# Performance work log

Measured on AMD Instinct MI355X. Metric: run time of the kernel, lower is better.

The kernel has to match this reference:

```python
import jax, jax.numpy as jnp
import numpy as np

GAMMA = 2.0
K_NEIGH = 10
N = 8192
F_IN = 512     # recon_fea_dim
F_HID = 512    # graph_h_dim
F_OUT = 256    # graph_out_dim
N_CLU = 10     # cluster_num


def setup_inputs() -> dict:
    key = jax.random.key(0)
    ks = jax.random.split(key, 8)
    x = jax.random.normal(ks[0], (N, F_IN), dtype=jnp.float32)
    # GCN layer 1 (selu activation, skip connection)
    W1 = jax.random.normal(ks[1], (F_IN, F_HID), dtype=jnp.float32) * (1.0 / np.sqrt(F_IN))
    b1 = jnp.zeros((F_HID,), dtype=jnp.float32)
    skip1 = jnp.ones((F_HID,), dtype=jnp.float32)
    # GCN layer 2 (identity activation, skip connection)
    W2 = jax.random.normal(ks[2], (F_HID, F_OUT), dtype=jnp.float32) * (1.0 / np.sqrt(F_HID))
    b2 = jnp.zeros((F_OUT,), dtype=jnp.float32)
    skip2 = jnp.ones((F_OUT,), dtype=jnp.float32)
    # MGC transform: Linear(graph_out_dim -> n_clusters)
    Wt = jax.random.normal(ks[3], (N_CLU, F_OUT), dtype=jnp.float32) * (1.0 / np.sqrt(F_OUT))
    bt = jnp.zeros((N_CLU,), dtype=jnp.float32)
    return {"x": x, "W1": W1, "b1": b1, "skip1": skip1,
            "W2": W2, "b2": b2, "skip2": skip2, "Wt": Wt, "bt": bt}


def _build_knn_graph(x):
    # pairwise squared distance via gram trick (same math as (x_i - x_j)**2 sum)
    sq = jnp.sum(x * x, axis=1)                       # [N]
    d2 = sq[:, None] + sq[None, :] - 2.0 * (x @ x.T)  # [N, N]
    S = jnp.exp(-d2 / GAMMA)
    S = jnp.where(jnp.eye(S.shape[0], dtype=bool), -jnp.inf, S)
    _, idx = jax.lax.top_k(S, K_NEIGH)                # [N, K]
    n = S.shape[0]
    rows = jnp.broadcast_to(jnp.arange(n)[:, None], idx.shape)
    A = jnp.zeros((n, n), dtype=jnp.float32)
    A = A.at[rows, idx].set(1.0)
    A = A.at[idx, rows].set(1.0)                      # symmetrize
    rowsum = jnp.sum(A, axis=1)
    inv = jnp.where(rowsum > 0, 1.0 / rowsum, 0.0)
    A_hat = A * inv[:, None]                          # D^{-1} A
    return A, A_hat


def _gcn_layer(h, A_hat, W, b, skip, act):
    out = h @ W
    out = out * skip + A_hat @ out                    # fused skip + aggregation
    out = out + b
    return act(out)


def reference(x, W1, b1, skip1, W2, b2, skip2, Wt, bt):
    A, A_hat = _build_knn_graph(x)
    # GCN encode: gc1 (selu) -> relu -> gc2 (identity)
    h = _gcn_layer(x, A_hat, W1, b1, skip1, jax.nn.selu)
    h = jax.nn.relu(h)
    emb = _gcn_layer(h, A_hat, W2, b2, skip2, lambda v: v)  # [N, F_OUT]
    # MGC spectral clustering loss
    assign = jax.nn.softmax(emb @ Wt.T + bt, axis=1)  # [N, C]
    deg = jnp.sum(A, axis=0)[:, None]                 # [N, 1]
    n_edges = jnp.sum(deg)
    graph_pooled = (A @ assign).T @ assign            # [C, C]
    norm_l = assign.T @ deg                           # [C, 1]
    norm_r = deg.T @ assign                           # [1, C]
    normalizer = (norm_l @ norm_r) / 2.0 / n_edges
    spectral_loss = -jnp.trace(graph_pooled - normalizer) / 2.0 / n_edges
    return spectral_loss
```

## Files before the change

kernel.cpp:

```cpp
#include <hip/hip_runtime.h>
#include <math.h>
#include <stdint.h>

#define NPTS 8192
#define FIN 512
#define FHID 512
#define FOUT 256
#define NCLU 10
#define KNEI 10
#define GAMMA_F 2.0f
#define LISTCAP 4160

typedef __attribute__((ext_vector_type(4))) float f32x4;
typedef __attribute__((ext_vector_type(8))) short bf16x8;

__global__ void k_sumsq(const float* __restrict__ x, float* __restrict__ sq) {
    int row = blockIdx.x;
    const float* xr = x + (size_t)row * FIN;
    float s = 0.f;
    for (int k = threadIdx.x; k < FIN; k += 256) s += xr[k] * xr[k];
    __shared__ float red[256];
    red[threadIdx.x] = s; __syncthreads();
    for (int off = 128; off > 0; off >>= 1) {
        if (threadIdx.x < off) red[threadIdx.x] += red[threadIdx.x + off];
        __syncthreads();
    }
    if (threadIdx.x == 0) sq[row] = red[0];
}

__global__ void k_tobf16(const float* __restrict__ x, unsigned short* __restrict__ xb) {
    int i = blockIdx.x * 256 + threadIdx.x;
    f32x4 v = reinterpret_cast<const f32x4*>(x)[i];
    ushort4 o;
    #pragma unroll
    for (int e = 0; e < 4; e++) {
        union { float f; unsigned u; } cvt; cvt.f = v[e];
        unsigned r = (cvt.u + 0x7FFFu + ((cvt.u >> 16) & 1u)) >> 16;
        ((unsigned short*)&o)[e] = (unsigned short)r;
    }
    reinterpret_cast<ushort4*>(xb)[i] = o;
}

#define GR_ROWS 64
#define GR_TW 128
#define GR_CHUNKS 8
#define GR_CHUNK_COLS (NPTS / GR_CHUNKS)
#define GR_TILES_PER_CHUNK (GR_CHUNK_COLS / GR_TW)
#define GR_STEPS (GR_TILES_PER_CHUNK * 8)

__global__ __launch_bounds__(256, 3) void k_gram_topk(
    const unsigned short* __restrict__ xb, const float* __restrict__ sq,
    float* __restrict__ tpv, int* __restrict__ tpi)
{
    __shared__ short Bl[2][128][64];
    __shared__ float tval[GR_ROWS][KNEI];
    __shared__ int   tidxs[GR_ROWS][KNEI];

    const int tid  = threadIdx.x;
    const int lane = tid & 63;
    const int wv   = tid >> 6;
    const int rg   = blockIdx.x >> 3;
    const int ch   = blockIdx.x & 7;
    const int r0   = rg * GR_ROWS;
    const int cbase = ch * GR_CHUNK_COLS;

    for (int e = tid; e < GR_ROWS * KNEI; e += 256) {
        tval[e / KNEI][e % KNEI] = -INFINITY;
        tidxs[e / KNEI][e % KNEI] = 0x7fffffff;
    }

    const int arow  = r0 + wv * 16 + (lane & 15);
    const int akoff = (lane >> 4) * 8;
    bf16x8 afr[16];
    #pragma unroll
    for (int ks = 0; ks < 16; ks++)
        afr[ks] = *reinterpret_cast<const bf16x8*>(xb + (size_t)arow * FIN + ks * 32 + akoff);

    float si_r[4];
    #pragma unroll
    for (int r = 0; r < 4; r++) si_r[r] = sq[r0 + wv * 16 + (lane >> 4) * 4 + r];

    const int stg_row = tid >> 1, stg_seg = tid & 1;

    bf16x8 pre[4];
    {
        const unsigned short* src = xb + (size_t)(cbase + stg_row) * FIN + stg_seg * 32;
        #pragma unroll
        for (int q = 0; q < 4; q++) pre[q] = *reinterpret_cast<const bf16x8*>(src + q * 8);
        #pragma unroll
        for (int q = 0; q < 4; q++) {
            int kk8 = stg_seg * 4 + q;
            *reinterpret_cast<bf16x8*>(&Bl[0][stg_row][(kk8 ^ (stg_row & 7)) * 8]) = pre[q];
        }
    }
    __syncthreads();

    f32x4 acc[8];
    for (int u = 0; u < GR_STEPS; ++u) {
        const int t  = u >> 3, kc = u & 7;
        const int c0 = cbase + t * GR_TW;
        const int cur = u & 1;

        if (kc == 0) {
            #pragma unroll
            for (int ct = 0; ct < 8; ct++) acc[ct] = (f32x4){0.f, 0.f, 0.f, 0.f};
        }

        if (u < GR_STEPS - 1) {
            const int u2 = u + 1, t2 = u2 >> 3, kc2 = u2 & 7;
            const unsigned short* src = xb + (size_t)(cbase + t2 * GR_TW + stg_row) * FIN + kc2 * 64 + stg_seg * 32;
            #pragma unroll
            for (int q = 0; q < 4; q++) pre[q] = *reinterpret_cast<const bf16x8*>(src + q * 8);
        }

        #pragma unroll
        for (int ksl = 0; ksl < 2; ++ksl) {
            #pragma unroll
            for (int ct = 0; ct < 8; ct++) {
                const int cl = ct * 16 + (lane & 15);
                const int q = ksl * 4 + (lane >> 4);
                bf16x8 bfr = *reinterpret_cast<const bf16x8*>(&Bl[cur][cl][(q ^ (cl & 7)) * 8]);
                acc[ct] = __builtin_amdgcn_mfma_f32_16x16x32_bf16(afr[kc * 2 + ksl], bfr, acc[ct], 0, 0, 0);
            }
        }

        if (kc == 7) {
            #pragma unroll
            for (int ct = 0; ct < 8; ct++) {
                const int gj  = c0 + ct * 16 + (lane & 15);
                const float sjv = sq[gj];
                float sv[4];
                #pragma unroll
                for (int r = 0; r < 4; r++) {
                    const int gi = r0 + wv * 16 + (lane >> 4) * 4 + r;
                    const float d2 = si_r[r] + sjv - 2.f * acc[ct][r];
                    sv[r] = (gj == gi) ? -INFINITY : expf(-d2 * 0.5f);
                }
                #pragma unroll
                for (int r = 0; r < 4; r++) {
                    const int myrow = wv * 16 + (lane >> 4) * 4 + r;
                    float t9 = tval[myrow][KNEI - 1];
                    int   i9 = tidxs[myrow][KNEI - 1];
                    unsigned long long bal = __ballot(sv[r] > t9 || (sv[r] == t9 && gj < i9));
                    while (bal) {
                        int l = __ffsll(bal) - 1;
                        bal &= bal - 1;
                        float cv = __shfl(sv[r], l);
                        int   cj = c0 + ct * 16 + (l & 15);
                        int   rfull = wv * 16 + (l >> 4) * 4 + r;
                        if (lane == 0) {
                            float a9 = tval[rfull][KNEI - 1];
                            int   i9b = tidxs[rfull][KNEI - 1];
                            if (cv > a9 || (cv == a9 && cj < i9b)) {
                                int pp = KNEI - 1;
                                tval[rfull][pp] = cv; tidxs[rfull][pp] = cj;
                                while (pp > 0) {
                                    float pv = tval[rfull][pp - 1]; int pi = tidxs[rfull][pp - 1];
                                    if (cv > pv || (cv == pv && cj < pi)) {
                                        tval[rfull][pp] = pv; tidxs[rfull][pp] = pi;
                                        tval[rfull][pp - 1] = cv; tidxs[rfull][pp - 1] = cj;
                                        --pp;
                                    } else break;
                                }
                            }
                        }
                    }
                }
            }
        }

        if (u < GR_STEPS - 1) {
            #pragma unroll
            for (int q = 0; q < 4; q++) {
                int kk8 = stg_seg * 4 + q;
                *reinterpret_cast<bf16x8*>(&Bl[cur ^ 1][stg_row][(kk8 ^ (stg_row & 7)) * 8]) = pre[q];
            }
        }
        __syncthreads();
    }

    for (int e = tid; e < GR_ROWS * KNEI; e += 256) {
        int r = e / KNEI, m = e % KNEI;
        size_t o = (((size_t)(r0 + r) * GR_CHUNKS) + ch) * KNEI + m;
        tpv[o] = tval[r][m];
        tpi[o] = tidxs[r][m];
    }
}

__global__ __launch_bounds__(256) void k_topk_merge(const float* __restrict__ tpv,
        const int* __restrict__ tpi, int* __restrict__ topidx) {
    int r = blockIdx.x * 256 + threadIdx.x;
    int p[GR_CHUNKS];
    #pragma unroll
    for (int c = 0; c < GR_CHUNKS; c++) p[c] = 0;
    #pragma unroll
    for (int m = 0; m < KNEI; m++) {
        float bv = -INFINITY; int bi = 0x7fffffff; int bc = 0;
        #pragma unroll
        for (int c = 0; c < GR_CHUNKS; c++) {
            if (p[c] < KNEI) {
                size_t o = (((size_t)r * GR_CHUNKS) + c) * KNEI + p[c];
                float v = tpv[o];
                int idx = tpi[o];
                if (v > bv || (v == bv && idx < bi)) { bv = v; bi = idx; bc = c; }
            }
        }
        topidx[(size_t)r * KNEI + m] = bi;
        p[bc]++;
    }
}

__global__ void k_set_edges(const int* __restrict__ topidx, unsigned int* __restrict__ mask) {
    int t = blockIdx.x * 256 + threadIdx.x;
    if (t >= NPTS * KNEI) return;
    int i = t / KNEI;
    int j = topidx[t];
    atomicOr(&mask[(size_t)i * (NPTS / 32) + (j >> 5)], 1u << (j & 31));
    atomicOr(&mask[(size_t)j * (NPTS / 32) + (i >> 5)], 1u << (i & 31));
}

__global__ void k_degree(const unsigned int* __restrict__ mask, float* __restrict__ degf,
                         float* __restrict__ inv) {
    int i = blockIdx.x, lane = threadIdx.x;
    int c = 0;
    for (int w = lane; w < NPTS / 32; w += 64) c += __popc(mask[(size_t)i * (NPTS / 32) + w]);
    for (int off = 32; off > 0; off >>= 1) c += __shfl_xor(c, off);
    if (lane == 0) {
        float d = (float)c;
        degf[i] = d;
        inv[i] = (c > 0) ? 1.0f / d : 0.0f;
    }
}

__global__ __launch_bounds__(256) void k_gemm(const float* __restrict__ A, const float* __restrict__ B,
                                              float* __restrict__ C, int M, int Kd, int Nd) {
    __shared__ float Al[64][17];
    __shared__ float Bl[16][65];
    int tid = threadIdx.x;
    int bx = blockIdx.x, by = blockIdx.y;
    int tx = tid & 15, ty = tid >> 4;
    float acc[4][4];
    #pragma unroll
    for (int i = 0; i < 4; i++)
        #pragma unroll
        for (int j = 0; j < 4; j++) acc[i][j] = 0.f;

    for (int kt = 0; kt < Kd; kt += 16) {
        #pragma unroll
        for (int l = 0; l < 4; l++) {
            int e = tid + l * 256;
            int r = e >> 4, k = e & 15;
            Al[r][k] = A[(size_t)(by * 64 + r) * Kd + kt + k];
        }
        #pragma unroll
        for (int l = 0; l < 4; l++) {
            int e = tid + l * 256;
            int r = e >> 6, n = e & 63;
            Bl[r][n] = B[(size_t)(kt + r) * Nd + bx * 64 + n];
        }
        __syncthreads();
        #pragma unroll
        for (int k = 0; k < 16; k++) {
            float a[4], b[4];
            #pragma unroll
            for (int i = 0; i < 4; i++) a[i] = Al[ty * 4 + i][k];
            #pragma unroll
            for (int j = 0; j < 4; j++) b[j] = Bl[k][tx * 4 + j];
            #pragma unroll
            for (int i = 0; i < 4; i++)
                #pragma unroll
                for (int j = 0; j < 4; j++) acc[i][j] = fmaf(a[i], b[j], acc[i][j]);
        }
        __syncthreads();
    }
    #pragma unroll
    for (int i = 0; i < 4; i++)
        #pragma unroll
        for (int j = 0; j < 4; j++)
            C[(size_t)(by * 64 + ty * 4 + i) * Nd + bx * 64 + tx * 4 + j] = acc[i][j];
}

__global__ __launch_bounds__(256) void k_colsum(const float* __restrict__ P, float* __restrict__ colsum, int Fd) {
    int f = blockIdx.x * 256 + threadIdx.x;
    int r0 = blockIdx.y * (NPTS / 64);
    float s = 0.f;
    for (int r = 0; r < NPTS / 64; r++) s += P[(size_t)(r0 + r) * Fd + f];
    atomicAdd(&colsum[f], s);
}

template <int ACT>
__global__ __launch_bounds__(256) void k_aggregate(const float* __restrict__ P, float* __restrict__ OUT,
        const float* __restrict__ skip, const float* __restrict__ bias,
        const float* __restrict__ inv, const unsigned int* __restrict__ mask,
        const float* __restrict__ colsum, int Fd) {
    __shared__ unsigned short list[LISTCAP];
    __shared__ int cnt_total;
    __shared__ int pos;
    int i = blockIdx.x, tid = threadIdx.x;
    if (tid == 0) { cnt_total = 0; pos = 0; }
    __syncthreads();
    unsigned int w = mask[(size_t)i * (NPTS / 32) + tid];
    atomicAdd(&cnt_total, __popc(w));
    __syncthreads();
    const int deg = cnt_total;
    const bool comp = deg > 4096;
    unsigned int wm = comp ? ~w : w;
    if (comp && tid == (i >> 5)) wm &= ~(1u << (i & 31));
    while (wm) {
        int b = __ffs(wm) - 1;
        wm &= wm - 1;
        int pp = atomicAdd(&pos, 1);
        list[pp] = (unsigned short)(tid * 32 + b);
    }
    __syncthreads();
    const int n = comp ? (NPTS - 1 - deg) : deg;
    const float vinv = inv[i];
    for (int f = tid; f < Fd; f += 256) {
        float s = 0.f;
        for (int q = 0; q < n; q++) s += P[(size_t)list[q] * Fd + f];
        const float pif = P[(size_t)i * Fd + f];
        const float nb = comp ? (colsum[f] - pif - s) : s;
        float o = pif * skip[f] + vinv * nb + bias[f];
        if (ACT == 1) o = (o > 0.f) ? 1.0507009873554805f * o : 0.f;
        OUT[(size_t)i * Fd + f] = o;
    }
}

__global__ void k_assign(const float* __restrict__ emb, const float* __restrict__ Wt,
                         const float* __restrict__ bt, float* __restrict__ assign) {
    int i = blockIdx.x, lane = threadIdx.x;
    float e[4];
    #pragma unroll
    for (int m = 0; m < 4; m++) e[m] = emb[(size_t)i * FOUT + lane + 64 * m];
    float logit[NCLU];
    #pragma unroll
    for (int c = 0; c < NCLU; c++) {
        float p = 0.f;
        #pragma unroll
        for (int m = 0; m < 4; m++) p = fmaf(e[m], Wt[c * FOUT + lane + 64 * m], p);
        #pragma unroll
        for (int off = 32; off > 0; off >>= 1) p += __shfl_xor(p, off);
        logit[c] = p + bt[c];
    }
    float mx = logit[0];
    #pragma unroll
    for (int c = 1; c < NCLU; c++) mx = fmaxf(mx, logit[c]);
    float sum = 0.f, pr[NCLU];
    #pragma unroll
    for (int c = 0; c < NCLU; c++) { pr[c] = expf(logit[c] - mx); sum += pr[c]; }
    float isum = 1.f / sum;
    if (lane < NCLU) {
        float v = 0.f;
        #pragma unroll
        for (int c = 0; c < NCLU; c++) if (lane == c) v = pr[c];
        assign[(size_t)i * NCLU + lane] = v * isum;
    }
}

__global__ __launch_bounds__(256) void k_stats(const float* __restrict__ assign,
        const float* __restrict__ degf, float* __restrict__ colA,
        float* __restrict__ vvec, float* __restrict__ Esum) {
    __shared__ float sc[NCLU], sv[NCLU], se;
    int tid = threadIdx.x;
    if (tid < NCLU) { sc[tid] = 0.f; sv[tid] = 0.f; }
    if (tid == 0) se = 0.f;
    __syncthreads();
    int i = blockIdx.x * 256 + tid;
    const float d = degf[i];
    const float* ar = assign + (size_t)i * NCLU;
    float ed = d;
    #pragma unroll
    for (int off = 32; off > 0; off >>= 1) ed += __shfl_xor(ed, off);
    if ((tid & 63) == 0) atomicAdd(&se, ed);
    #pragma unroll
    for (int c = 0; c < NCLU; c++) {
        float a = ar[c];
        float av = a * d;
        #pragma unroll
        for (int off = 32; off > 0; off >>= 1) { a += __shfl_xor(a, off); av += __shfl_xor(av, off); }
        if ((tid & 63) == 0) { atomicAdd(&sc[c], a); atomicAdd(&sv[c], av); }
    }
    __syncthreads();
    if (tid < NCLU) { atomicAdd(&colA[tid], sc[tid]); atomicAdd(&vvec[tid], sv[tid]); }
    if (tid == NCLU) atomicAdd(Esum, se);
}

__global__ __launch_bounds__(256) void k_spectral(const unsigned int* __restrict__ mask,
        const float* __restrict__ assign, const float* __restrict__ colA,
        float* __restrict__ Tpart) {
    __shared__ unsigned short list[LISTCAP];
    __shared__ int cnt_total;
    __shared__ int pos;
    __shared__ float red[4][NCLU];
    int i = blockIdx.x, tid = threadIdx.x;
    if (tid == 0) { cnt_total = 0; pos = 0; }
    __syncthreads();
    unsigned int w = mask[(size_t)i * (NPTS / 32) + tid];
    atomicAdd(&cnt_total, __popc(w));
    __syncthreads();
    const int deg = cnt_total;
    const bool comp = deg > 4096;
    unsigned int wm = comp ? ~w : w;
    if (comp && tid == (i >> 5)) wm &= ~(1u << (i & 31));
    while (wm) {
        int b = __ffs(wm) - 1;
        wm &= wm - 1;
        int pp = atomicAdd(&pos, 1);
        list[pp] = (unsigned short)(tid * 32 + b);
    }
    __syncthreads();
    const int n = comp ? (NPTS - 1 - deg) : deg;
    float yc[NCLU];
    #pragma unroll
    for (int c = 0; c < NCLU; c++) yc[c] = 0.f;
    for (int q = tid; q < n; q += 256) {
        const float* aj = assign + (size_t)list[q] * NCLU;
        #pragma unroll
        for (int c = 0; c < NCLU; c++) yc[c] += aj[c];
    }
    #pragma unroll
    for (int c = 0; c < NCLU; c++) {
        #pragma unroll
        for (int off = 32; off > 0; off >>= 1) yc[c] += __shfl_xor(yc[c], off);
    }
    int wv = tid >> 6, lane = tid & 63;
    if (lane == 0) {
        #pragma unroll
        for (int c = 0; c < NCLU; c++) red[wv][c] = yc[c];
    }
    __syncthreads();
    if (tid == 0) {
        const float* ai = assign + (size_t)i * NCLU;
        float t = 0.f;
        #pragma unroll
        for (int c = 0; c < NCLU; c++) {
            float y = red[0][c] + red[1][c] + red[2][c] + red[3][c];
            if (comp) y = colA[c] - ai[c] - y;
            t = fmaf(y, ai[c], t);
        }
        Tpart[i] = t;
    }
}

__global__ __launch_bounds__(256) void k_final(const float* __restrict__ Tpart,
        const float* __restrict__ v, const float* __restrict__ Esum, float* __restrict__ out) {
    __shared__ float red[256];
    int tid = threadIdx.x;
    float s = 0.f;
    for (int i = tid; i < NPTS; i += 256) s += Tpart[i];
    red[tid] = s; __syncthreads();
    for (int off = 128; off > 0; off >>= 1) {
        if (tid < off) red[tid] += red[tid + off];
        __syncthreads();
    }
    if (tid == 0) {
        float E = *Esum;
        float v2 = 0.f;
        for (int c = 0; c < NCLU; c++) v2 += v[c] * v[c];
        float tr_norm = v2 / (2.f * E);
        out[0] = -(red[0] - tr_norm) / (2.f * E);
    }
}

extern "C" void kernel_launch(void* const* d_in, const int* in_sizes, int n_in,
                              void* d_out, int out_size, void* d_ws, size_t ws_size,
                              hipStream_t stream) {
    const float* x     = (const float*)d_in[0];
    const float* W1    = (const float*)d_in[1];
    const float* b1    = (const float*)d_in[2];
    const float* skip1 = (const float*)d_in[3];
    const float* W2    = (const float*)d_in[4];
    const float* b2    = (const float*)d_in[5];
    const float* skip2 = (const float*)d_in[6];
    const float* Wt    = (const float*)d_in[7];
    const float* bt    = (const float*)d_in[8];

    char* ws = (char*)d_ws;
    float* bufA = (float*)ws;
    float* bufB = (float*)(ws + ((size_t)16 << 20));
    unsigned int* mask = (unsigned int*)(ws + ((size_t)32 << 20));
    char* p = ws + ((size_t)40 << 20);
    float* sq     = (float*)p; p += NPTS * 4;
    float* degf   = (float*)p; p += NPTS * 4;
    float* inv    = (float*)p; p += NPTS * 4;
    int*   topidx = (int*)p;   p += (size_t)NPTS * KNEI * 4;
    float* assign = (float*)p; p += (size_t)NPTS * NCLU * 4;
    float* Tpart  = (float*)p; p += NPTS * 4;
    float* Esum    = (float*)p; p += 4;
    float* vvec    = (float*)p; p += NCLU * 4;
    float* colA    = (float*)p; p += NCLU * 4;
    float* colsum1 = (float*)p; p += FHID * 4;
    float* colsum2 = (float*)p; p += FOUT * 4;

    unsigned short* xb = (unsigned short*)bufA;
    float* tpv = (float*)bufB;
    int*   tpi = (int*)((char*)bufB + ((size_t)4 << 20));

    hipMemsetAsync(mask, 0, (size_t)NPTS * (NPTS / 32) * 4, stream);
    hipMemsetAsync(Esum, 0, (1 + 2 * NCLU + FHID + FOUT) * sizeof(float), stream);

    k_sumsq<<<NPTS, 256, 0, stream>>>(x, sq);
    k_tobf16<<<(NPTS * FIN / 4) / 256, 256, 0, stream>>>(x, xb);
    k_gram_topk<<<(NPTS / GR_ROWS) * GR_CHUNKS, 256, 0, stream>>>(xb, sq, tpv, tpi);
    k_topk_merge<<<NPTS / 256, 256, 0, stream>>>(tpv, tpi, topidx);
    k_set_edges<<<(NPTS * KNEI + 255) / 256, 256, 0, stream>>>(topidx, mask);
    k_degree<<<NPTS, 64, 0, stream>>>(mask, degf, inv);

    k_gemm<<<dim3(FHID / 64, NPTS / 64), 256, 0, stream>>>(x, W1, bufA, NPTS, FIN, FHID);
    k_colsum<<<dim3(FHID / 256, 64), 256, 0, stream>>>(bufA, colsum1, FHID);
    k_aggregate<1><<<NPTS, 256, 0, stream>>>(bufA, bufB, skip1, b1, inv, mask, colsum1, FHID);
    k_gemm<<<dim3(FOUT / 64, NPTS / 64), 256, 0, stream>>>(bufB, W2, bufA, NPTS, FHID, FOUT);
    k_colsum<<<dim3(FOUT / 256, 64), 256, 0, stream>>>(bufA, colsum2, FOUT);
    k_aggregate<0><<<NPTS, 256, 0, stream>>>(bufA, bufB, skip2, b2, inv, mask, colsum2, FOUT);

    k_assign<<<NPTS, 64, 0, stream>>>(bufB, Wt, bt, assign);
    k_stats<<<NPTS / 256, 256, 0, stream>>>(assign, degf, colA, vvec, Esum);
    k_spectral<<<NPTS, 256, 0, stream>>>(mask, assign, colA, Tpart);
    k_final<<<1, 256, 0, stream>>>(Tpart, vvec, Esum, (float*)d_out);
}
```

Before: 728.8 us.

## Use split-bf16 MFMA GEMMs for GCN layers and enlarge gram-topk row tile

The scalar fp32 shared-memory GEMMs for both GCN layers are replaced by an MFMA kernel. Each fp32 operand is split into high and low bf16 parts, and three bf16 MFMA products (hi*hi, hi*lo, lo*hi) give near-fp32 accuracy. New helper kernels split the activations and transpose and split the weights; B fragments are read directly from global memory with no LDS staging. Separately, the gram/top-k kernel now processes 128 rows per block with 512 threads, which amortizes B-tile staging over more rows. In exchange there are extra split passes, a dropped lo*lo term, and different occupancy in the gram kernel.

```diff
diff --git a/kernel.cpp b/kernel.cpp
--- a/kernel.cpp
+++ b/kernel.cpp
@@ -8,11 +8,19 @@
 #define FOUT 256
 #define NCLU 10
 #define KNEI 10
-#define GAMMA_F 2.0f
 #define LISTCAP 4160
 
 typedef __attribute__((ext_vector_type(4))) float f32x4;
 typedef __attribute__((ext_vector_type(8))) short bf16x8;
+
+__device__ __forceinline__ unsigned short bf16_rne(float f) {
+    union { float f; unsigned u; } c; c.f = f;
+    return (unsigned short)((c.u + 0x7FFFu + ((c.u >> 16) & 1u)) >> 16);
+}
+__device__ __forceinline__ float bf16_to_f(unsigned short h) {
+    union { unsigned u; float f; } c; c.u = ((unsigned)h) << 16;
+    return c.f;
+}
 
 __global__ void k_sumsq(const float* __restrict__ x, float* __restrict__ sq) {
     int row = blockIdx.x;
@@ -28,27 +36,48 @@
     if (threadIdx.x == 0) sq[row] = red[0];
 }
 
-__global__ void k_tobf16(const float* __restrict__ x, unsigned short* __restrict__ xb) {
+__global__ void k_split(const float* __restrict__ in, unsigned short* __restrict__ hi,
+                        unsigned short* __restrict__ lo) {
     int i = blockIdx.x * 256 + threadIdx.x;
-    f32x4 v = reinterpret_cast<const f32x4*>(x)[i];
-    ushort4 o;
+    f32x4 v = reinterpret_cast<const f32x4*>(in)[i];
+    ushort4 h, l;
     #pragma unroll
     for (int e = 0; e < 4; e++) {
-        union { float f; unsigned u; } cvt; cvt.f = v[e];
-        unsigned r = (cvt.u + 0x7FFFu + ((cvt.u >> 16) & 1u)) >> 16;
-        ((unsigned short*)&o)[e] = (unsigned short)r;
-    }
-    reinterpret_cast<ushort4*>(xb)[i] = o;
-}
-
-#define GR_ROWS 64
+        unsigned short hb = bf16_rne(v[e]);
+        ((unsigned short*)&h)[e] = hb;
+        ((unsigned short*)&l)[e] = bf16_rne(v[e] - bf16_to_f(hb));
+    }
+    reinterpret_cast<ushort4*>(hi)[i] = h;
+    reinterpret_cast<ushort4*>(lo)[i] = l;
+}
+
+__global__ __launch_bounds__(256) void k_wtrans(const float* __restrict__ W,
+        unsigned short* __restrict__ TH, unsigned short* __restrict__ TL, int K, int N) {
+    __shared__ float t[32][33];
+    int k0 = blockIdx.y * 32, n0 = blockIdx.x * 32;
+    int ln = threadIdx.x & 31, lt = threadIdx.x >> 5;
+    #pragma unroll
+    for (int q = 0; q < 4; q++)
+        t[lt + q * 8][ln] = W[(size_t)(k0 + lt + q * 8) * N + n0 + ln];
+    __syncthreads();
+    #pragma unroll
+    for (int q = 0; q < 4; q++) {
+        float v = t[ln][lt + q * 8];
+        unsigned short hb = bf16_rne(v);
+        size_t o = (size_t)(n0 + lt + q * 8) * K + k0 + ln;
+        TH[o] = hb;
+        TL[o] = bf16_rne(v - bf16_to_f(hb));
+    }
+}
+
+#define GR_ROWS 128
 #define GR_TW 128
 #define GR_CHUNKS 8
 #define GR_CHUNK_COLS (NPTS / GR_CHUNKS)
 #define GR_TILES_PER_CHUNK (GR_CHUNK_COLS / GR_TW)
 #define GR_STEPS (GR_TILES_PER_CHUNK * 8)
 
-__global__ __launch_bounds__(256, 3) void k_gram_topk(
+__global__ __launch_bounds__(512, 2) void k_gram_topk(
     const unsigned short* __restrict__ xb, const float* __restrict__ sq,
     float* __restrict__ tpv, int* __restrict__ tpi)
 {
@@ -64,7 +93,7 @@
     const int r0   = rg * GR_ROWS;
     const int cbase = ch * GR_CHUNK_COLS;
 
-    for (int e = tid; e < GR_ROWS * KNEI; e += 256) {
+    for (int e = tid; e < GR_ROWS * KNEI; e += 512) {
         tval[e / KNEI][e % KNEI] = -INFINITY;
         tidxs[e / KNEI][e % KNEI] = 0x7fffffff;
     }
@@ -80,17 +109,17 @@
     #pragma unroll
     for (int r = 0; r < 4; r++) si_r[r] = sq[r0 + wv * 16 + (lane >> 4) * 4 + r];
 
-    const int stg_row = tid >> 1, stg_seg = tid & 1;
-
-    bf16x8 pre[4];
+    const int stg_row = tid >> 2, stg_seg = tid & 3;
+
+    bf16x8 pre[2];
     {
-        const unsigned short* src = xb + (size_t)(cbase + stg_row) * FIN + stg_seg * 32;
-        #pragma unroll
-        for (int q = 0; q < 4; q++) pre[q] = *reinterpret_cast<const bf16x8*>(src + q * 8);
-        #pragma unroll
-        for (int q = 0; q < 4; q++) {
-            int kk8 = stg_seg * 4 + q;
-            *reinterpret_cast<bf16x8*>(&Bl[0][stg_row][(kk8 ^ (stg_row & 7)) * 8]) = pre[q];
+        const unsigned short* src = xb + (size_t)(cbase + stg_row) * FIN + stg_seg * 16;
+        #pragma unroll
+        for (int q = 0; q < 2; q++) pre[q] = *reinterpret_cast<const bf16x8*>(src + q * 8);
+        #pragma unroll
+        for (int q = 0; q < 2; q++) {
+            int g = stg_seg * 2 + q;
+            *reinterpret_cast<bf16x8*>(&Bl[0][stg_row][(g ^ (stg_row & 7)) * 8]) = pre[q];
         }
     }
     __syncthreads();
@@ -108,9 +137,9 @@
 
         if (u < GR_STEPS - 1) {
             const int u2 = u + 1, t2 = u2 >> 3, kc2 = u2 & 7;
-            const unsigned short* src = xb + (size_t)(cbase + t2 * GR_TW + stg_row) * FIN + kc2 * 64 + stg_seg * 32;
+            const unsigned short* src = xb + (size_t)(cbase + t2 * GR_TW + stg_row) * FIN + kc2 * 64 + stg_seg * 16;
             #pragma unroll
-            for (int q = 0; q < 4; q++) pre[q] = *reinterpret_cast<const bf16x8*>(src + q * 8);
+            for (int q = 0; q < 2; q++) pre[q] = *reinterpret_cast<const bf16x8*>(src + q * 8);
         }
 
         #pragma unroll
@@ -171,15 +200,15 @@
 
         if (u < GR_STEPS - 1) {
             #pragma unroll
-            for (int q = 0; q < 4; q++) {
-                int kk8 = stg_seg * 4 + q;
-                *reinterpret_cast<bf16x8*>(&Bl[cur ^ 1][stg_row][(kk8 ^ (stg_row & 7)) * 8]) = pre[q];
+            for (int q = 0; q < 2; q++) {
+                int g = stg_seg * 2 + q;
+                *reinterpret_cast<bf16x8*>(&Bl[cur ^ 1][stg_row][(g ^ (stg_row & 7)) * 8]) = pre[q];
             }
         }
         __syncthreads();
     }
 
-    for (int e = tid; e < GR_ROWS * KNEI; e += 256) {
+    for (int e = tid; e < GR_ROWS * KNEI; e += 512) {
         int r = e / KNEI, m = e % KNEI;
         size_t o = (((size_t)(r0 + r) * GR_CHUNKS) + ch) * KNEI + m;
         tpv[o] = tval[r][m];
@@ -232,52 +261,49 @@
     }
 }
 
-__global__ __launch_bounds__(256) void k_gemm(const float* __restrict__ A, const float* __restrict__ B,
-                                              float* __restrict__ C, int M, int Kd, int Nd) {
-    __shared__ float Al[64][17];
-    __shared__ float Bl[16][65];
-    int tid = threadIdx.x;
-    int bx = blockIdx.x, by = blockIdx.y;
-    int tx = tid & 15, ty = tid >> 4;
-    float acc[4][4];
-    #pragma unroll
-    for (int i = 0; i < 4; i++)
-        #pragma unroll
-        for (int j = 0; j < 4; j++) acc[i][j] = 0.f;
-
-    for (int kt = 0; kt < Kd; kt += 16) {
-        #pragma unroll
-        for (int l = 0; l < 4; l++) {
-            int e = tid + l * 256;
-            int r = e >> 4, k = e & 15;
-            Al[r][k] = A[(size_t)(by * 64 + r) * Kd + kt + k];
-        }
-        #pragma unroll
-        for (int l = 0; l < 4; l++) {
-            int e = tid + l * 256;
-            int r = e >> 6, n = e & 63;
-            Bl[r][n] = B[(size_t)(kt + r) * Nd + bx * 64 + n];
-        }
-        __syncthreads();
-        #pragma unroll
-        for (int k = 0; k < 16; k++) {
-            float a[4], b[4];
+__global__ __launch_bounds__(256) void k_gemm_mfma(
+    const unsigned short* __restrict__ Ahi, const unsigned short* __restrict__ Alo,
+    const unsigned short* __restrict__ BThi, const unsigned short* __restrict__ BTlo,
+    float* __restrict__ C, int M, int K, int N)
+{
+    const int tid = threadIdx.x, lane = tid & 63, wv = tid >> 6;
+    const int bx = blockIdx.x, by = blockIdx.y;
+    const int arow = by * 64 + wv * 16 + (lane & 15);
+    const int koff = (lane >> 4) * 8;
+
+    f32x4 acc[8];
+    #pragma unroll
+    for (int ct = 0; ct < 8; ct++) acc[ct] = (f32x4){0.f, 0.f, 0.f, 0.f};
+
+    for (int kb = 0; kb < K; kb += 128) {
+        bf16x8 ah[4], al[4];
+        #pragma unroll
+        for (int ksl = 0; ksl < 4; ksl++) {
+            ah[ksl] = *reinterpret_cast<const bf16x8*>(Ahi + (size_t)arow * K + kb + ksl * 32 + koff);
+            al[ksl] = *reinterpret_cast<const bf16x8*>(Alo + (size_t)arow * K + kb + ksl * 32 + koff);
+        }
+        #pragma unroll
+        for (int ksl = 0; ksl < 4; ksl++) {
             #pragma unroll
-            for (int i = 0; i < 4; i++) a[i] = Al[ty * 4 + i][k];
-            #pragma unroll
-            for (int j = 0; j < 4; j++) b[j] = Bl[k][tx * 4 + j];
-            #pragma unroll
-            for (int i = 0; i < 4; i++)
-                #pragma unroll
-                for (int j = 0; j < 4; j++) acc[i][j] = fmaf(a[i], b[j], acc[i][j]);
-        }
-        __syncthreads();
-    }
-    #pragma unroll
-    for (int i = 0; i < 4; i++)
-        #pragma unroll
-        for (int j = 0; j < 4; j++)
-            C[(size_t)(by * 64 + ty * 4 + i) * Nd + bx * 64 + tx * 4 + j] = acc[i][j];
+            for (int ct = 0; ct < 8; ct++) {
+                const int n = bx * 128 + ct * 16 + (lane & 15);
+                bf16x8 bh = *reinterpret_cast<const bf16x8*>(BThi + (size_t)n * K + kb + ksl * 32 + koff);
+                bf16x8 bl = *reinterpret_cast<const bf16x8*>(BTlo + (size_t)n * K + kb + ksl * 32 + koff);
+                acc[ct] = __builtin_amdgcn_mfma_f32_16x16x32_bf16(ah[ksl], bh, acc[ct], 0, 0, 0);
+                acc[ct] = __builtin_amdgcn_mfma_f32_16x16x32_bf16(ah[ksl], bl, acc[ct], 0, 0, 0);
+                acc[ct] = __builtin_amdgcn_mfma_f32_16x16x32_bf16(al[ksl], bh, acc[ct], 0, 0, 0);
+            }
+        }
+    }
+    #pragma unroll
+    for (int ct = 0; ct < 8; ct++) {
+        const int col = bx * 128 + ct * 16 + (lane & 15);
+        #pragma unroll
+        for (int r = 0; r < 4; r++) {
+            const int row = by * 64 + wv * 16 + (lane >> 4) * 4 + r;
+            C[(size_t)row * N + col] = acc[ct][r];
+        }
+    }
 }
 
 __global__ __launch_bounds__(256) void k_colsum(const float* __restrict__ P, float* __restrict__ colsum, int Fd) {
@@ -479,7 +505,8 @@
     float* bufA = (float*)ws;
     float* bufB = (float*)(ws + ((size_t)16 << 20));
     unsigned int* mask = (unsigned int*)(ws + ((size_t)32 << 20));
-    char* p = ws + ((size_t)40 << 20);
+    unsigned short* xlo = (unsigned short*)(ws + ((size_t)40 << 20));
+    char* p = ws + ((size_t)48 << 20);
     float* sq     = (float*)p; p += NPTS * 4;
     float* degf   = (float*)p; p += NPTS * 4;
     float* inv    = (float*)p; p += NPTS * 4;
@@ -491,29 +518,40 @@
     float* colA    = (float*)p; p += NCLU * 4;
     float* colsum1 = (float*)p; p += FHID * 4;
     float* colsum2 = (float*)p; p += FOUT * 4;
+    unsigned short* WT1hi = (unsigned short*)p; p += (size_t)FHID * FIN * 2;
+    unsigned short* WT1lo = (unsigned short*)p; p += (size_t)FHID * FIN * 2;
+    unsigned short* WT2hi = (unsigned short*)p; p += (size_t)FOUT * FHID * 2;
+    unsigned short* WT2lo = (unsigned short*)p; p += (size_t)FOUT * FHID * 2;
 
     unsigned short* xb = (unsigned short*)bufA;
     float* tpv = (float*)bufB;
     int*   tpi = (int*)((char*)bufB + ((size_t)4 << 20));
+    unsigned short* hhi = (unsigned short*)bufB;
+    float* P2 = bufB + ((size_t)2 << 20);
 
     hipMemsetAsync(mask, 0, (size_t)NPTS * (NPTS / 32) * 4, stream);
     hipMemsetAsync(Esum, 0, (1 + 2 * NCLU + FHID + FOUT) * sizeof(float), stream);
 
     k_sumsq<<<NPTS, 256, 0, stream>>>(x, sq);
-    k_tobf16<<<(NPTS * FIN / 4) / 256, 256, 0, stream>>>(x, xb);
-    k_gram_topk<<<(NPTS / GR_ROWS) * GR_CHUNKS, 256, 0, stream>>>(xb, sq, tpv, tpi);
+    k_split<<<(NPTS * FIN / 4) / 256, 256, 0, stream>>>(x, xb, xlo);
+    k_wtrans<<<dim3(FHID / 32, FIN / 32), 256, 0, stream>>>(W1, WT1hi, WT1lo, FIN, FHID);
+    k_wtrans<<<dim3(FOUT / 32, FHID / 32), 256, 0, stream>>>(W2, WT2hi, WT2lo, FHID, FOUT);
+
+    k_gram_topk<<<(NPTS / GR_ROWS) * GR_CHUNKS, 512, 0, stream>>>(xb, sq, tpv, tpi);
     k_topk_merge<<<NPTS / 256, 256, 0, stream>>>(tpv, tpi, topidx);
     k_set_edges<<<(NPTS * KNEI + 255) / 256, 256, 0, stream>>>(topidx, mask);
     k_degree<<<NPTS, 64, 0, stream>>>(mask, degf, inv);
 
-    k_gemm<<<dim3(FHID / 64, NPTS / 64), 256, 0, stream>>>(x, W1, bufA, NPTS, FIN, FHID);
-    k_colsum<<<dim3(FHID / 256, 64), 256, 0, stream>>>(bufA, colsum1, FHID);
-    k_aggregate<1><<<NPTS, 256, 0, stream>>>(bufA, bufB, skip1, b1, inv, mask, colsum1, FHID);
-    k_gemm<<<dim3(FOUT / 64, NPTS / 64), 256, 0, stream>>>(bufB, W2, bufA, NPTS, FHID, FOUT);
-    k_colsum<<<dim3(FOUT / 256, 64), 256, 0, stream>>>(bufA, colsum2, FOUT);
-    k_aggregate<0><<<NPTS, 256, 0, stream>>>(bufA, bufB, skip2, b2, inv, mask, colsum2, FOUT);
-
-    k_assign<<<NPTS, 64, 0, stream>>>(bufB, Wt, bt, assign);
+    k_gemm_mfma<<<dim3(FHID / 128, NPTS / 64), 256, 0, stream>>>(xb, xlo, WT1hi, WT1lo, bufB, NPTS, FIN, FHID);
+    k_colsum<<<dim3(FHID / 256, 64), 256, 0, stream>>>(bufB, colsum1, FHID);
+    k_aggregate<1><<<NPTS, 256, 0, stream>>>(bufB, bufA, skip1, b1, inv, mask, colsum1, FHID);
+
+    k_split<<<(NPTS * FHID / 4) / 256, 256, 0, stream>>>(bufA, hhi, xlo);
+    k_gemm_mfma<<<dim3(FOUT / 128, NPTS / 64), 256, 0, stream>>>(hhi, xlo, WT2hi, WT2lo, P2, NPTS, FHID, FOUT);
+    k_colsum<<<dim3(FOUT / 256, 64), 256, 0, stream>>>(P2, colsum2, FOUT);
+    k_aggregate<0><<<NPTS, 256, 0, stream>>>(P2, bufA, skip2, b2, inv, mask, colsum2, FOUT);
+
+    k_assign<<<NPTS, 64, 0, stream>>>(bufA, Wt, bt, assign);
     k_stats<<<NPTS / 256, 256, 0, stream>>>(assign, degf, colA, vvec, Esum);
     k_spectral<<<NPTS, 256, 0, stream>>>(mask, assign, colA, Tpart);
     k_final<<<1, 256, 0, stream>>>(Tpart, vvec, Esum, (float*)d_out);
```

New measurement: 720.7 us. About the same (-1.1%).
